# Kernel tuning notes

Hardware: AMD Instinct MI355X
Metric: run time of the kernel (lower is better)

The kernel has to match this reference:

```python
import jax, jax.numpy as jnp
import numpy as np

NV, P, C, H, O = 50000, 32, 4, 64, 128
EPS = 1e-5


def _bn(x, g, b, m, v):
    # inference-mode BatchNorm1d over channel dim
    return (x - m) * jax.lax.rsqrt(v + EPS) * g + b


def setup_inputs() -> dict:
    key = jax.random.key(0)
    ks = jax.random.split(key, 16)
    voxel_features = jax.random.normal(ks[0], (NV, P, C), jnp.float32)
    voxel_num_points = jax.random.randint(ks[1], (NV,), 1, P + 1).astype(jnp.int64)
    def lin(k, fin, fout):
        kw, kb = jax.random.split(k)
        s = 1.0 / np.sqrt(fin)
        W = jax.random.uniform(kw, (fin, fout), jnp.float32, -s, s)
        b = jax.random.uniform(kb, (fout,), jnp.float32, -s, s)
        return W, b
    W1, b1 = lin(ks[2], C, H)
    W2, b2 = lin(ks[3], H, H)
    W3, b3 = lin(ks[4], H, O)
    g1 = jax.random.uniform(ks[5], (H,), jnp.float32, 0.5, 1.5)
    be1 = jax.random.normal(ks[6], (H,), jnp.float32) * 0.1
    m1 = jax.random.normal(ks[7], (H,), jnp.float32) * 0.1
    v1 = jax.random.uniform(ks[8], (H,), jnp.float32, 0.5, 1.5)
    g2 = jax.random.uniform(ks[9], (H,), jnp.float32, 0.5, 1.5)
    be2 = jax.random.normal(ks[10], (H,), jnp.float32) * 0.1
    m2 = jax.random.normal(ks[11], (H,), jnp.float32) * 0.1
    v2 = jax.random.uniform(ks[12], (H,), jnp.float32, 0.5, 1.5)
    return dict(voxel_features=voxel_features, voxel_num_points=voxel_num_points,
                W1=W1, b1=b1, g1=g1, be1=be1, m1=m1, v1=v1,
                W2=W2, b2=b2, g2=g2, be2=be2, m2=m2, v2=v2,
                W3=W3, b3=b3)


def reference(voxel_features, voxel_num_points,
              W1, b1, g1, be1, m1, v1,
              W2, b2, g2, be2, m2, v2,
              W3, b3):
    nv, p, c = voxel_features.shape
    x = voxel_features.reshape(-1, c)                 # (NV*P, C)
    x = jax.nn.relu(_bn(x @ W1 + b1, g1, be1, m1, v1))
    x = jax.nn.relu(_bn(x @ W2 + b2, g2, be2, m2, v2))
    x = x @ W3 + b3                                   # (NV*P, O)
    x = x.reshape(nv, p, -1)
    mask = jnp.arange(p)[None, :] < voxel_num_points[:, None]  # (NV, P)
    # original multiplies by mask then masked-fills -inf; net effect is -inf fill
    x = jnp.where(mask[:, :, None], x, -jnp.inf)
    return jnp.max(x, axis=1)                         # (NV, O)
```

## Files before the change

### kernel.cpp

```cpp
#include <hip/hip_runtime.h>
#include <math.h>

#define NVOX 50000
#define PPTS 32
#define HDIM 64
#define ODIM 128
#define EPSBN 1e-5f

#define RS 72

typedef _Float16 f16x8 __attribute__((ext_vector_type(8)));
typedef _Float16 f16x4 __attribute__((ext_vector_type(4)));
typedef float f32x4 __attribute__((ext_vector_type(4)));

#define WS_W1C 0
#define WS_W2T 512
#define WS_W3T 4608
#define WS_F32_BYTE 25600
#define FOLD_THREADS 12992

__global__ void vfe_fold(
    const float* __restrict__ W1, const float* __restrict__ b1,
    const float* __restrict__ g1, const float* __restrict__ be1,
    const float* __restrict__ m1, const float* __restrict__ v1,
    const float* __restrict__ W2, const float* __restrict__ b2,
    const float* __restrict__ g2, const float* __restrict__ be2,
    const float* __restrict__ m2, const float* __restrict__ v2,
    const float* __restrict__ W3, const float* __restrict__ b3,
    _Float16* __restrict__ wsh, float* __restrict__ wsf)
{
    int t = blockIdx.x * 256 + threadIdx.x;
    if (t < 512) {
        int row = t >> 3, i = t & 7;
        float s1 = g1[row] * rsqrtf(v1[row] + EPSBN);
        float val;
        if (i < 4)      val = W1[i * 64 + row] * s1;
        else if (i == 4) val = (b1[row] - m1[row]) * s1 + be1[row];
        else             val = 0.f;
        wsh[WS_W1C + t] = (_Float16)val;
    } else if (t < 4608) {
        int e = t - 512;
        int chp = e >> 6, ch = e & 63;
        float s2 = g2[chp] * rsqrtf(v2[chp] + EPSBN);
        wsh[t] = (_Float16)(W2[ch * 64 + chp] * s2);
    } else if (t < 12800) {
        int e = t - 4608;
        int o = e >> 6, ch = e & 63;
        wsh[t] = (_Float16)W3[ch * 128 + o];
    } else if (t < 12864) {
        int i = t - 12800;
        float s2 = g2[i] * rsqrtf(v2[i] + EPSBN);
        wsf[i] = (b2[i] - m2[i]) * s2 + be2[i];
    } else if (t < FOLD_THREADS) {
        int i = t - 12864;
        wsf[64 + i] = b3[i];
    }
}

__global__ __launch_bounds__(256, 3) void vfe_mfma(
    const float* __restrict__ vf, const int* __restrict__ vnp,
    const _Float16* __restrict__ wsh, const float* __restrict__ wsf,
    float* __restrict__ out)
{
    __shared__ __align__(16) _Float16 sH[4][4][16 * RS];
    __shared__ __align__(16) _Float16 sW3[ODIM * HDIM];

    const int tid  = threadIdx.x;
    const int wave = tid >> 6;
    const int lane = tid & 63;
    const int q    = lane >> 4;
    const int m16  = lane & 15;

    const int wavebase = blockIdx.x * 256 + wave * 64;
    const int voxA = wavebase >> 5;

#pragma unroll
    for (int i = 0; i < 4; ++i) {
        int G = tid + 256 * i;
        int o = G >> 3, gl = G & 7;
        int ph = gl ^ (o & 7);
        f16x8 v = *(const f16x8*)&wsh[WS_W3T + o * 64 + gl * 8];
        *(f16x8*)&sW3[o * 64 + ph * 8] = v;
    }

    const int nA = vnp[voxA];
    const int nB = vnp[voxA + 1];

    f16x8 a1[4];
#pragma unroll
    for (int mt = 0; mt < 4; ++mt) {
        f16x8 t = *(const f16x8*)&wsh[WS_W1C + (m16 + 16 * mt) * 8];
        a1[mt] = (q == 0) ? t : (f16x8)0;
    }
    f16x8 a2[4][2];
#pragma unroll
    for (int mt = 0; mt < 4; ++mt)
#pragma unroll
        for (int kk = 0; kk < 2; ++kk)
            a2[mt][kk] = *(const f16x8*)&wsh[WS_W2T + (m16 + 16 * mt) * 64 + kk * 32 + q * 8];
    f32x4 c2v[4];
#pragma unroll
    for (int mt = 0; mt < 4; ++mt)
        c2v[mt] = *(const f32x4*)(wsf + mt * 16 + q * 4);
    float b3r[8];
#pragma unroll
    for (int nt = 0; nt < 8; ++nt) b3r[nt] = wsf[64 + nt * 16 + m16];

    float4 xv[4];
#pragma unroll
    for (int g = 0; g < 4; ++g)
        xv[g] = *(const float4*)(vf + ((size_t)wavebase + g * 16 + m16) * 4);

    f16x8 bf[4];
#pragma unroll
    for (int g = 0; g < 4; ++g) {
        f16x8 b = (f16x8)0;
        if (q == 0) {
            b[0] = (_Float16)xv[g].x; b[1] = (_Float16)xv[g].y;
            b[2] = (_Float16)xv[g].z; b[3] = (_Float16)xv[g].w;
            b[4] = (_Float16)1.0f;
        }
        bf[g] = b;
    }

    __syncthreads();

#pragma unroll
    for (int g = 0; g < 4; ++g) {
        _Float16* ht = &sH[wave][g][0];
#pragma unroll
        for (int mt = 0; mt < 4; ++mt) {
            f32x4 acc = {0.f, 0.f, 0.f, 0.f};
            acc = __builtin_amdgcn_mfma_f32_16x16x32_f16(a1[mt], bf[g], acc, 0, 0, 0);
            f16x4 h;
            h[0] = (_Float16)fmaxf(acc[0], 0.f);
            h[1] = (_Float16)fmaxf(acc[1], 0.f);
            h[2] = (_Float16)fmaxf(acc[2], 0.f);
            h[3] = (_Float16)fmaxf(acc[3], 0.f);
            *(f16x4*)&ht[m16 * RS + mt * 16 + q * 4] = h;
        }
    }

    f16x8 b2f[4][2];
#pragma unroll
    for (int g = 0; g < 4; ++g) {
        _Float16* ht = &sH[wave][g][0];
        b2f[g][0] = *(const f16x8*)&ht[m16 * RS + q * 8];
        b2f[g][1] = *(const f16x8*)&ht[m16 * RS + 32 + q * 8];
    }
#pragma unroll
    for (int g = 0; g < 4; ++g) {
        _Float16* ht = &sH[wave][g][0];
#pragma unroll
        for (int mt = 0; mt < 4; ++mt) {
            f32x4 acc = c2v[mt];
            acc = __builtin_amdgcn_mfma_f32_16x16x32_f16(a2[mt][0], b2f[g][0], acc, 0, 0, 0);
            acc = __builtin_amdgcn_mfma_f32_16x16x32_f16(a2[mt][1], b2f[g][1], acc, 0, 0, 0);
            f16x4 h;
            h[0] = (_Float16)fmaxf(acc[0], 0.f);
            h[1] = (_Float16)fmaxf(acc[1], 0.f);
            h[2] = (_Float16)fmaxf(acc[2], 0.f);
            h[3] = (_Float16)fmaxf(acc[3], 0.f);
            *(f16x4*)&ht[m16 * RS + mt * 16 + q * 4] = h;
        }
    }

    f16x8 a3[4][2];
#pragma unroll
    for (int g = 0; g < 4; ++g) {
        _Float16* ht = &sH[wave][g][0];
        a3[g][0] = *(const f16x8*)&ht[m16 * RS + q * 8];
        a3[g][1] = *(const f16x8*)&ht[m16 * RS + 32 + q * 8];
    }

    f32x4 macc4[4];
#pragma unroll
    for (int g = 0; g < 4; ++g) {
        const int n = (g < 2) ? nA : nB;
        const int slotbase = (g & 1) * 16 + q * 4;
#pragma unroll
        for (int r = 0; r < 4; ++r)
            macc4[g][r] = (slotbase + r < n) ? 0.f : -INFINITY;
    }

    float vmA[8], vmB[8];
#pragma unroll
    for (int nt = 0; nt < 8; ++nt) { vmA[nt] = -INFINITY; vmB[nt] = -INFINITY; }

#pragma unroll
    for (int nt = 0; nt < 8; ++nt) {
        const int o = nt * 16 + m16;
        f16x8 b30 = *(const f16x8*)&sW3[o * 64 + ((q    ) ^ (m16 & 7)) * 8];
        f16x8 b31 = *(const f16x8*)&sW3[o * 64 + ((4 + q) ^ (m16 & 7)) * 8];
#pragma unroll
        for (int g = 0; g < 4; ++g) {
            f32x4 acc = macc4[g];
            acc = __builtin_amdgcn_mfma_f32_16x16x32_f16(a3[g][0], b30, acc, 0, 0, 0);
            acc = __builtin_amdgcn_mfma_f32_16x16x32_f16(a3[g][1], b31, acc, 0, 0, 0);
            float m0 = fmaxf(fmaxf(acc[0], acc[1]), fmaxf(acc[2], acc[3]));
            if (g < 2) vmA[nt] = fmaxf(vmA[nt], m0);
            else       vmB[nt] = fmaxf(vmB[nt], m0);
        }
    }

#pragma unroll
    for (int nt = 0; nt < 8; ++nt) {
        float t0 = vmA[nt];
        t0 = fmaxf(t0, __shfl_xor(t0, 16));
        t0 = fmaxf(t0, __shfl_xor(t0, 32));
        float t1 = vmB[nt];
        t1 = fmaxf(t1, __shfl_xor(t1, 16));
        t1 = fmaxf(t1, __shfl_xor(t1, 32));
        if (q == 0) out[(size_t)(voxA + 0) * ODIM + nt * 16 + m16] = t0 + b3r[nt];
        if (q == 1) out[(size_t)(voxA + 1) * ODIM + nt * 16 + m16] = t1 + b3r[nt];
    }
}

extern "C" void kernel_launch(void* const* d_in, const int* in_sizes, int n_in,
                              void* d_out, int out_size, void* d_ws, size_t ws_size,
                              hipStream_t stream) {
    const float* vf  = (const float*)d_in[0];
    const int*   vnp = (const int*)d_in[1];
    const float* W1  = (const float*)d_in[2];
    const float* b1  = (const float*)d_in[3];
    const float* g1  = (const float*)d_in[4];
    const float* be1 = (const float*)d_in[5];
    const float* m1  = (const float*)d_in[6];
    const float* v1  = (const float*)d_in[7];
    const float* W2  = (const float*)d_in[8];
    const float* b2  = (const float*)d_in[9];
    const float* g2  = (const float*)d_in[10];
    const float* be2 = (const float*)d_in[11];
    const float* m2  = (const float*)d_in[12];
    const float* v2  = (const float*)d_in[13];
    const float* W3  = (const float*)d_in[14];
    const float* b3  = (const float*)d_in[15];
    float* out = (float*)d_out;

    _Float16* wsh = (_Float16*)d_ws;
    float*    wsf = (float*)((char*)d_ws + WS_F32_BYTE);

    vfe_fold<<<(FOLD_THREADS + 255) / 256, 256, 0, stream>>>(
        W1, b1, g1, be1, m1, v1, W2, b2, g2, be2, m2, v2, W3, b3, wsh, wsf);

    const int blocks = (NVOX * PPTS) / 256;
    vfe_mfma<<<blocks, 256, 0, stream>>>(vf, vnp, wsh, wsf, out);
}
```

Measured before the change: 167.3 us.

## Permute hidden channels so MFMA outputs feed next layer in registers

Reorders the hidden channels in the folded W1/W2 weights and bias so that each MFMA accumulator layout matches the operand layout needed by the next MFMA. The per-wave LDS staging of hidden activations between layers is removed. Occupancy hint is raised from 3 to 4 blocks per CU, the input load is restricted to lanes that use it, and the b3 load is deferred to lower register pressure. The risk is register spills under the tighter launch bound, plus correctness depending on the permutation matching the lane layout.

```diff
diff --git a/kernel.cpp b/kernel.cpp
--- a/kernel.cpp
+++ b/kernel.cpp
@@ -7,8 +7,6 @@
 #define ODIM 128
 #define EPSBN 1e-5f
 
-#define RS 72
-
 typedef _Float16 f16x8 __attribute__((ext_vector_type(8)));
 typedef _Float16 f16x4 __attribute__((ext_vector_type(4)));
 typedef float f32x4 __attribute__((ext_vector_type(4)));
@@ -18,6 +16,10 @@
 #define WS_W3T 4608
 #define WS_F32_BYTE 25600
 #define FOLD_THREADS 12992
+
+__device__ __host__ inline int permch(int p) {
+    return ((p >> 4) & 1) * 32 + ((p >> 2) & 3) * 8 + ((p >> 5) & 1) * 4 + (p & 3);
+}
 
 __global__ void vfe_fold(
     const float* __restrict__ W1, const float* __restrict__ b1,
@@ -31,16 +33,18 @@
 {
     int t = blockIdx.x * 256 + threadIdx.x;
     if (t < 512) {
-        int row = t >> 3, i = t & 7;
-        float s1 = g1[row] * rsqrtf(v1[row] + EPSBN);
+        int p = t >> 3, i = t & 7;
+        int ch = permch(p);
+        float s1 = g1[ch] * rsqrtf(v1[ch] + EPSBN);
         float val;
-        if (i < 4)      val = W1[i * 64 + row] * s1;
-        else if (i == 4) val = (b1[row] - m1[row]) * s1 + be1[row];
+        if (i < 4)      val = W1[i * 64 + ch] * s1;
+        else if (i == 4) val = (b1[ch] - m1[ch]) * s1 + be1[ch];
         else             val = 0.f;
         wsh[WS_W1C + t] = (_Float16)val;
     } else if (t < 4608) {
         int e = t - 512;
-        int chp = e >> 6, ch = e & 63;
+        int p = e >> 6, ch = e & 63;
+        int chp = permch(p);
         float s2 = g2[chp] * rsqrtf(v2[chp] + EPSBN);
         wsh[t] = (_Float16)(W2[ch * 64 + chp] * s2);
     } else if (t < 12800) {
@@ -57,12 +61,11 @@
     }
 }
 
-__global__ __launch_bounds__(256, 3) void vfe_mfma(
+__global__ __launch_bounds__(256, 4) void vfe_mfma(
     const float* __restrict__ vf, const int* __restrict__ vnp,
     const _Float16* __restrict__ wsh, const float* __restrict__ wsf,
     float* __restrict__ out)
 {
-    __shared__ __align__(16) _Float16 sH[4][4][16 * RS];
     __shared__ __align__(16) _Float16 sW3[ODIM * HDIM];
 
     const int tid  = threadIdx.x;
@@ -101,17 +104,17 @@
     f32x4 c2v[4];
 #pragma unroll
     for (int mt = 0; mt < 4; ++mt)
-        c2v[mt] = *(const f32x4*)(wsf + mt * 16 + q * 4);
-    float b3r[8];
-#pragma unroll
-    for (int nt = 0; nt < 8; ++nt) b3r[nt] = wsf[64 + nt * 16 + m16];
+        c2v[mt] = *(const f32x4*)(wsf + (mt & 1) * 32 + q * 8 + (mt >> 1) * 4);
 
     float4 xv[4];
 #pragma unroll
     for (int g = 0; g < 4; ++g)
-        xv[g] = *(const float4*)(vf + ((size_t)wavebase + g * 16 + m16) * 4);
-
-    f16x8 bf[4];
+        if (q == 0)
+            xv[g] = *(const float4*)(vf + ((size_t)wavebase + g * 16 + m16) * 4);
+
+    __syncthreads();
+
+    f16x8 a3[4][2];
 #pragma unroll
     for (int g = 0; g < 4; ++g) {
         f16x8 b = (f16x8)0;
@@ -120,57 +123,35 @@
             b[2] = (_Float16)xv[g].z; b[3] = (_Float16)xv[g].w;
             b[4] = (_Float16)1.0f;
         }
-        bf[g] = b;
-    }
-
-    __syncthreads();
-
-#pragma unroll
-    for (int g = 0; g < 4; ++g) {
-        _Float16* ht = &sH[wave][g][0];
+        f32x4 p1[4];
 #pragma unroll
         for (int mt = 0; mt < 4; ++mt) {
-            f32x4 acc = {0.f, 0.f, 0.f, 0.f};
-            acc = __builtin_amdgcn_mfma_f32_16x16x32_f16(a1[mt], bf[g], acc, 0, 0, 0);
-            f16x4 h;
-            h[0] = (_Float16)fmaxf(acc[0], 0.f);
-            h[1] = (_Float16)fmaxf(acc[1], 0.f);
-            h[2] = (_Float16)fmaxf(acc[2], 0.f);
-            h[3] = (_Float16)fmaxf(acc[3], 0.f);
-            *(f16x4*)&ht[m16 * RS + mt * 16 + q * 4] = h;
-        }
-    }
-
-    f16x8 b2f[4][2];
-#pragma unroll
-    for (int g = 0; g < 4; ++g) {
-        _Float16* ht = &sH[wave][g][0];
-        b2f[g][0] = *(const f16x8*)&ht[m16 * RS + q * 8];
-        b2f[g][1] = *(const f16x8*)&ht[m16 * RS + 32 + q * 8];
-    }
-#pragma unroll
-    for (int g = 0; g < 4; ++g) {
-        _Float16* ht = &sH[wave][g][0];
+            f32x4 z = {0.f, 0.f, 0.f, 0.f};
+            p1[mt] = __builtin_amdgcn_mfma_f32_16x16x32_f16(a1[mt], b, z, 0, 0, 0);
+        }
+        f16x8 b20, b21;
+#pragma unroll
+        for (int r = 0; r < 4; ++r) {
+            b20[r]     = (_Float16)fmaxf(p1[0][r], 0.f);
+            b20[4 + r] = (_Float16)fmaxf(p1[2][r], 0.f);
+            b21[r]     = (_Float16)fmaxf(p1[1][r], 0.f);
+            b21[4 + r] = (_Float16)fmaxf(p1[3][r], 0.f);
+        }
+        f32x4 p2[4];
 #pragma unroll
         for (int mt = 0; mt < 4; ++mt) {
             f32x4 acc = c2v[mt];
-            acc = __builtin_amdgcn_mfma_f32_16x16x32_f16(a2[mt][0], b2f[g][0], acc, 0, 0, 0);
-            acc = __builtin_amdgcn_mfma_f32_16x16x32_f16(a2[mt][1], b2f[g][1], acc, 0, 0, 0);
-            f16x4 h;
-            h[0] = (_Float16)fmaxf(acc[0], 0.f);
-            h[1] = (_Float16)fmaxf(acc[1], 0.f);
-            h[2] = (_Float16)fmaxf(acc[2], 0.f);
-            h[3] = (_Float16)fmaxf(acc[3], 0.f);
-            *(f16x4*)&ht[m16 * RS + mt * 16 + q * 4] = h;
-        }
-    }
-
-    f16x8 a3[4][2];
-#pragma unroll
-    for (int g = 0; g < 4; ++g) {
-        _Float16* ht = &sH[wave][g][0];
-        a3[g][0] = *(const f16x8*)&ht[m16 * RS + q * 8];
-        a3[g][1] = *(const f16x8*)&ht[m16 * RS + 32 + q * 8];
+            acc = __builtin_amdgcn_mfma_f32_16x16x32_f16(a2[mt][0], b20, acc, 0, 0, 0);
+            acc = __builtin_amdgcn_mfma_f32_16x16x32_f16(a2[mt][1], b21, acc, 0, 0, 0);
+            p2[mt] = acc;
+        }
+#pragma unroll
+        for (int r = 0; r < 4; ++r) {
+            a3[g][0][r]     = (_Float16)fmaxf(p2[0][r], 0.f);
+            a3[g][0][4 + r] = (_Float16)fmaxf(p2[2][r], 0.f);
+            a3[g][1][r]     = (_Float16)fmaxf(p2[1][r], 0.f);
+            a3[g][1][4 + r] = (_Float16)fmaxf(p2[3][r], 0.f);
+        }
     }
 
     f32x4 macc4[4];
@@ -202,6 +183,10 @@
             else       vmB[nt] = fmaxf(vmB[nt], m0);
         }
     }
+
+    float b3r[8];
+#pragma unroll
+    for (int nt = 0; nt < 8; ++nt) b3r[nt] = wsf[64 + nt * 16 + m16];
 
 #pragma unroll
     for (int nt = 0; nt < 8; ++nt) {
```

After: 239.6 us. 1.43x slower.
